# Performance work log

Measured on AMD Instinct MI355X. Metric: run time of the kernel, lower is better.

## Reference

```python
import jax, jax.numpy as jnp
import numpy as np

N_NODES = 32768
N_EDGES = 524288
NODE_DIM = 128
HIDDEN = 256
EDGE_DIM = 32


def setup_inputs() -> dict:
    key = jax.random.key(0)
    ks = jax.random.split(key, 12)
    s = 0.05
    return {
        "h": jax.random.normal(ks[0], (N_NODES, NODE_DIM), jnp.float32),
        "x": jax.random.normal(ks[1], (N_NODES, 3), jnp.float32) * 10.0,
        "edge_index": jax.random.randint(ks[2], (2, N_EDGES), 0, N_NODES, dtype=jnp.int32).astype(jnp.int64),
        "edge_dist": jax.random.uniform(ks[3], (N_EDGES,), jnp.float32) * 15.0,
        # edge_mlp: Linear(1, edge_dim) -> SiLU -> Linear(edge_dim, edge_dim)
        "We1": jax.random.normal(ks[4], (1, EDGE_DIM), jnp.float32) * s,
        "be1": jnp.zeros((EDGE_DIM,), jnp.float32),
        "We2": jax.random.normal(ks[5], (EDGE_DIM, EDGE_DIM), jnp.float32) * s,
        "be2": jnp.zeros((EDGE_DIM,), jnp.float32),
        # node_mlp: Linear(2*node+edge, hidden) -> SiLU -> Linear(hidden, node)
        "Wn1": jax.random.normal(ks[6], (2 * NODE_DIM + EDGE_DIM, HIDDEN), jnp.float32) * s,
        "bn1": jnp.zeros((HIDDEN,), jnp.float32),
        "Wn2": jax.random.normal(ks[7], (HIDDEN, NODE_DIM), jnp.float32) * s,
        "bn2": jnp.zeros((NODE_DIM,), jnp.float32),
        # coord_mlp: Linear(2*node+edge, hidden) -> SiLU -> Linear(hidden, 1, bias=False)
        "Wc1": jax.random.normal(ks[8], (2 * NODE_DIM + EDGE_DIM, HIDDEN), jnp.float32) * s,
        "bc1": jnp.zeros((HIDDEN,), jnp.float32),
        "Wc2": jax.random.normal(ks[9], (HIDDEN, 1), jnp.float32) * s,
    }


def reference(h, x, edge_index, edge_dist,
              We1, be1, We2, be2,
              Wn1, bn1, Wn2, bn2,
              Wc1, bc1, Wc2):
    src, dst = edge_index[0], edge_index[1]
    n_nodes = h.shape[0]

    # edge_mlp on scalar distances -> [E, edge_dim]
    edge_attr = jax.nn.silu(edge_dist[:, None] @ We1 + be1) @ We2 + be2

    # per-edge message input: [E, 2*node_dim + edge_dim]
    m_input = jnp.concatenate([h[src], h[dst], edge_attr], axis=-1)

    # node messages and scatter-add onto destination nodes
    m = jax.nn.silu(m_input @ Wn1 + bn1) @ Wn2 + bn2          # [E, node_dim]
    h_agg = jax.ops.segment_sum(m, dst, num_segments=n_nodes)  # [N, node_dim]

    # equivariant coordinate update along normalized edge direction
    coord_weight = jax.nn.silu(m_input @ Wc1 + bc1) @ Wc2      # [E, 1]
    dir_vec = x[src] - x[dst]                                  # [E, 3]
    dir_len = jnp.maximum(jnp.linalg.norm(dir_vec, axis=-1, keepdims=True), 1e-8)
    coord_update = coord_weight * (dir_vec / dir_len)          # [E, 3]
    x_agg = jax.ops.segment_sum(coord_update, dst, num_segments=n_nodes)

    return h + h_agg, x + x_agg
```

## Files before the change

kernel.cpp:

```cpp
#include <hip/hip_runtime.h>
#include <math.h>

#define N_NODES 32768
#define N_EDGES 524288
#define NODE_DIM 128
#define HIDDEN 256
#define EDGE_DIM 32
#define TE 64
#define ASTR 296
#define HSTR 264
#define MSTR 132

typedef __attribute__((ext_vector_type(8))) short bf16x8;
typedef __attribute__((ext_vector_type(16))) float f32x16;

__device__ __forceinline__ float silu_f(float v) {
    float e = __expf(-v);
    return v * __builtin_amdgcn_rcpf(1.0f + e);
}

__device__ __forceinline__ unsigned short f2bf_rne(float f) {
    union { float f; unsigned int u; } v; v.f = f;
    return (unsigned short)((v.u + 0x7fffu + ((v.u >> 16) & 1u)) >> 16);
}

__device__ __forceinline__ unsigned int pkbf(float a, float b) {
    union { float f; unsigned int u; } ua, ub; ua.f = a; ub.f = b;
    return __builtin_amdgcn_perm(ub.u + 0x8000u, ua.u + 0x8000u, 0x07060302u);
}
__device__ __forceinline__ unsigned short f2bf_hu(float f) {
    union { float f; unsigned int u; } v; v.f = f;
    return (unsigned short)((v.u + 0x8000u) >> 16);
}

#define WS_BIAS_OFF 1024
#define WS_W1S_OFF  69632
#define WS_W2S_OFF  364544
#define WS_CNT_OFF  430080
#define WS_CUR_OFF  561152
#define WS_PERM_OFF 692224

__global__ void detect_zero_kernel(const unsigned int* __restrict__ ew, int* __restrict__ flag,
                                   int* __restrict__ counts) {
    int i = blockIdx.x * 256 + threadIdx.x;
    if (i < N_NODES) counts[i] = 0;
    if (i == 0) {
        int is64 = 1;
        for (int k = 0; k < 64; ++k)
            if (ew[2 * k + 1] != 0u) { is64 = 0; break; }
        *flag = is64;
    }
}

__global__ void hist_kernel(const void* __restrict__ ei, const int* __restrict__ flag,
                            int* __restrict__ counts) {
    int e = blockIdx.x * 256 + threadIdx.x;
    int dst = (*flag) ? (int)((const long long*)ei)[N_EDGES + e]
                      : ((const int*)ei)[N_EDGES + e];
    atomicAdd(&counts[dst], 1);
}

__global__ __launch_bounds__(1024)
void scan_kernel(const int* __restrict__ counts, int* __restrict__ cursor) {
    __shared__ int part[1024];
    const int t = threadIdx.x;
    const int base = t * 32;
    int loc[32];
    int s = 0;
    #pragma unroll
    for (int i = 0; i < 32; ++i) { loc[i] = s; s += counts[base + i]; }
    part[t] = s;
    __syncthreads();
    #pragma unroll
    for (int d = 1; d < 1024; d <<= 1) {
        int v = (t >= d) ? part[t - d] : 0;
        __syncthreads();
        part[t] += v;
        __syncthreads();
    }
    int excl = part[t] - s;
    #pragma unroll
    for (int i = 0; i < 32; ++i) cursor[base + i] = excl + loc[i];
}

__global__ void place_kernel(const void* __restrict__ ei, const int* __restrict__ flag,
                             int* __restrict__ cursor, int* __restrict__ perm) {
    int e = blockIdx.x * 256 + threadIdx.x;
    int dst = (*flag) ? (int)((const long long*)ei)[N_EDGES + e]
                      : ((const int*)ei)[N_EDGES + e];
    int pos = atomicAdd(&cursor[dst], 1);
    perm[pos] = e;
}

__global__ void init_out_kernel(const float4* __restrict__ h4, const float4* __restrict__ x4,
                                float4* __restrict__ out4) {
    const int NH4 = N_NODES * NODE_DIM / 4;
    const int NX4 = N_NODES * 3 / 4;
    int i = blockIdx.x * blockDim.x + threadIdx.x;
    if (i < NH4) out4[i] = h4[i];
    else if (i < NH4 + NX4) out4[i] = x4[i - NH4];
}

__global__ void prep_kernel(const float* __restrict__ Wn1, const float* __restrict__ Wc1,
                            const float* __restrict__ Wn2,
                            const float* __restrict__ bn1, const float* __restrict__ bc1,
                            const float* __restrict__ We2, const float* __restrict__ be2,
                            unsigned short* __restrict__ W1s, unsigned short* __restrict__ W2s,
                            float* __restrict__ biasC) {
    int i = blockIdx.x * 256 + threadIdx.x;
    if (i < 512 * 288) {
        int jj = i & 7, lane = (i >> 3) & 63, rest = i >> 9;
        int step = rest % 18, tile = rest / 18;
        int n = tile * 32 + (lane & 31);
        int k = step * 16 + ((lane >> 5) * 8) + jj;
        float v;
        if (k < 256) {
            v = (n < 256) ? Wn1[k * 256 + n] : Wc1[k * 256 + (n - 256)];
        } else {
            int j = k - 256;
            float s = 0.0f;
            #pragma unroll 8
            for (int q = 0; q < 32; ++q)
                s += We2[j * 32 + q] * ((n < 256) ? Wn1[(256 + q) * 256 + n]
                                                  : Wc1[(256 + q) * 256 + (n - 256)]);
            v = s;
        }
        W1s[i] = f2bf_rne(v);
    } else if (i < 512 * 288 + 128 * 256) {
        int i2 = i - 512 * 288;
        int jj = i2 & 7, lane = (i2 >> 3) & 63, rest = i2 >> 9;
        int step = rest & 15, tile = rest >> 4;
        int d = tile * 32 + (lane & 31);
        int k = step * 16 + ((lane >> 5) * 8) + jj;
        W2s[i2] = f2bf_rne(Wn2[k * 128 + d]);
    } else if (i < 512 * 288 + 128 * 256 + 512) {
        int n = i - (512 * 288 + 128 * 256);
        float s = (n < 256) ? bn1[n] : bc1[n - 256];
        #pragma unroll 8
        for (int q = 0; q < 32; ++q)
            s += be2[q] * ((n < 256) ? Wn1[(256 + q) * 256 + n]
                                     : Wc1[(256 + q) * 256 + (n - 256)]);
        biasC[n] = s;
    }
}

__global__ __launch_bounds__(512, 4)
void egnn_mfma_kernel(const float* __restrict__ h, const float* __restrict__ x,
                      const void* __restrict__ ei, const float* __restrict__ dist,
                      const float* __restrict__ We1, const float* __restrict__ be1,
                      const float* __restrict__ bn2, const float* __restrict__ Wc2,
                      const float* __restrict__ biasC,
                      const unsigned short* __restrict__ W1s,
                      const unsigned short* __restrict__ W2s,
                      const int* __restrict__ perm,
                      const int* __restrict__ flag,
                      float* __restrict__ out)
{
    __shared__ unsigned short smA[TE * ASTR];
    __shared__ int sidx[TE], didx[TE], eidx[TE];
    __shared__ float cw_s[TE];
    __shared__ float cxyz[3 * TE];

    unsigned short* smH = smA;
    float* smM = (float*)smA;

    const int t = threadIdx.x;
    const int lane = t & 63;
    const int wv = t >> 6;
    const int lo = lane & 31;
    const int hi = lane >> 5;
    const int ebase = blockIdx.x * TE;
    const int is64 = *flag;

    if (t < 2 * TE) {
        int e = t & (TE - 1);
        int eid = perm[ebase + e];
        int which = t >> 6;
        long long pos = (long long)which * N_EDGES + eid;
        int idx = is64 ? (int)((const long long*)ei)[pos] : ((const int*)ei)[pos];
        if (which == 0) { sidx[e] = idx; eidx[e] = eid; }
        else didx[e] = idx;
        if (t < TE) cw_s[t] = 0.0f;
    }
    __syncthreads();

    #pragma unroll
    for (int it = 0; it < 4; ++it) {
        int id = it * 512 + t;
        int g8 = id & 15;
        int half = (id >> 4) & 1;
        int e = id >> 5;
        int node = half ? didx[e] : sidx[e];
        const float4* p = (const float4*)&h[node * NODE_DIM + 8 * g8];
        float4 v0 = p[0], v1 = p[1];
        unsigned int a0 = pkbf(v0.x, v0.y), a1 = pkbf(v0.z, v0.w);
        unsigned int a2 = pkbf(v1.x, v1.y), a3 = pkbf(v1.z, v1.w);
        *(uint4*)&smA[e * ASTR + half * NODE_DIM + 8 * g8] = make_uint4(a0, a1, a2, a3);
    }
    {
        int e = t >> 3;
        int j4 = (t & 7) * 4;
        float d = dist[eidx[e]];
        float s0 = silu_f(d * We1[j4 + 0] + be1[j4 + 0]);
        float s1 = silu_f(d * We1[j4 + 1] + be1[j4 + 1]);
        float s2 = silu_f(d * We1[j4 + 2] + be1[j4 + 2]);
        float s3 = silu_f(d * We1[j4 + 3] + be1[j4 + 3]);
        *(uint2*)&smA[e * ASTR + 2 * NODE_DIM + j4] = make_uint2(pkbf(s0, s1), pkbf(s2, s3));
    }
    __syncthreads();

    f32x16 a00, a01, a10, a11;
    {
        int nb = wv * 64 + lo;
        float b0 = biasC[nb], b1 = biasC[nb + 32];
        #pragma unroll
        for (int r = 0; r < 16; ++r) { a00[r] = b0; a01[r] = b1; a10[r] = b0; a11[r] = b1; }
    }
    {
        const int aoff0 = lo * ASTR + hi * 8;
        const int aoff1 = (32 + lo) * ASTR + hi * 8;
        const int TS = 18 * 64 * 8;
        const int base = ((wv * 2 * 18) * 64 + lane) * 8;
        bf16x8 b0c = *(const bf16x8*)&W1s[base];
        bf16x8 b1c = *(const bf16x8*)&W1s[base + TS];
        #pragma unroll
        for (int step = 0; step < 18; ++step) {
            bf16x8 b0n, b1n;
            if (step < 17) {
                b0n = *(const bf16x8*)&W1s[base + (step + 1) * 512];
                b1n = *(const bf16x8*)&W1s[base + (step + 1) * 512 + TS];
            }
            bf16x8 f0 = *(const bf16x8*)&smA[aoff0 + step * 16];
            bf16x8 f1 = *(const bf16x8*)&smA[aoff1 + step * 16];
            a00 = __builtin_amdgcn_mfma_f32_32x32x16_bf16(f0, b0c, a00, 0, 0, 0);
            a10 = __builtin_amdgcn_mfma_f32_32x32x16_bf16(f1, b0c, a10, 0, 0, 0);
            a01 = __builtin_amdgcn_mfma_f32_32x32x16_bf16(f0, b1c, a01, 0, 0, 0);
            a11 = __builtin_amdgcn_mfma_f32_32x32x16_bf16(f1, b1c, a11, 0, 0, 0);
            if (step < 17) { b0c = b0n; b1c = b1n; }
        }
    }
    __syncthreads();

    const int rowbase = 4 * hi;
    if (wv < 4) {
        int jb = wv * 64 + lo;
        #pragma unroll
        for (int r = 0; r < 16; ++r) {
            int er = (r & 3) + 8 * (r >> 2) + rowbase;
            unsigned short* row0 = &smH[er * HSTR + jb];
            unsigned short* row1 = &smH[(er + 32) * HSTR + jb];
            row0[0]  = f2bf_hu(silu_f(a00[r]));
            row0[32] = f2bf_hu(silu_f(a01[r]));
            row1[0]  = f2bf_hu(silu_f(a10[r]));
            row1[32] = f2bf_hu(silu_f(a11[r]));
        }
    } else {
        int nc = (wv - 4) * 64 + lo;
        float w0 = Wc2[nc], w1 = Wc2[nc + 32];
        float p0[16], p1[16];
        #pragma unroll
        for (int r = 0; r < 16; ++r) {
            p0[r] = silu_f(a00[r]) * w0 + silu_f(a01[r]) * w1;
            p1[r] = silu_f(a10[r]) * w0 + silu_f(a11[r]) * w1;
        }
        #pragma unroll
        for (int off = 1; off < 32; off <<= 1) {
            #pragma unroll
            for (int r = 0; r < 16; ++r) {
                p0[r] += __shfl_xor(p0[r], off);
                p1[r] += __shfl_xor(p1[r], off);
            }
        }
        if (lo == 0) {
            #pragma unroll
            for (int r = 0; r < 16; ++r) {
                int er = (r & 3) + 8 * (r >> 2) + rowbase;
                atomicAdd(&cw_s[er], p0[r]);
                atomicAdd(&cw_s[er + 32], p1[r]);
            }
        }
    }
    __syncthreads();

    if (t < TE) {
        int s = sidx[t], dn = didx[t];
        float dx = x[s * 3 + 0] - x[dn * 3 + 0];
        float dy = x[s * 3 + 1] - x[dn * 3 + 1];
        float dz = x[s * 3 + 2] - x[dn * 3 + 2];
        float len = fmaxf(sqrtf(dx * dx + dy * dy + dz * dz), 1e-8f);
        float w = cw_s[t] / len;
        cxyz[t] = w * dx; cxyz[TE + t] = w * dy; cxyz[2 * TE + t] = w * dz;
    }

    {
        const int et = wv >> 2;
        const int dt = wv & 3;
        const int d = dt * 32 + lo;
        f32x16 acc;
        float b = bn2[d];
        #pragma unroll
        for (int r = 0; r < 16; ++r) acc[r] = b;
        const int hoff = (et * 32 + lo) * HSTR + hi * 8;
        const int wb = ((dt * 16) * 64 + lane) * 8;
        bf16x8 bc = *(const bf16x8*)&W2s[wb];
        #pragma unroll
        for (int step = 0; step < 16; ++step) {
            bf16x8 bn_;
            if (step < 15) bn_ = *(const bf16x8*)&W2s[wb + (step + 1) * 512];
            bf16x8 af = *(const bf16x8*)&smH[hoff + step * 16];
            acc = __builtin_amdgcn_mfma_f32_32x32x16_bf16(af, bc, acc, 0, 0, 0);
            if (step < 15) bc = bn_;
        }
        __syncthreads();
        #pragma unroll
        for (int r = 0; r < 16; ++r) {
            int er = et * 32 + (r & 3) + 8 * (r >> 2) + rowbase;
            smM[er * MSTR + d] = acc[r];
        }
    }
    __syncthreads();

    {
        const int g = t >> 5;
        const int d4 = (t & 31) * 4;
        for (int e0 = g; e0 < TE; e0 += 16) {
            if (e0 > 0 && didx[e0] == didx[e0 - 1]) continue;
            float4 s = *(const float4*)&smM[e0 * MSTR + d4];
            int er = e0 + 1;
            while (er < TE && didx[er] == didx[e0]) {
                float4 v = *(const float4*)&smM[er * MSTR + d4];
                s.x += v.x; s.y += v.y; s.z += v.z; s.w += v.w;
                ++er;
            }
            float* dp = &out[didx[e0] * NODE_DIM + d4];
            atomicAdd(dp + 0, s.x); atomicAdd(dp + 1, s.y);
            atomicAdd(dp + 2, s.z); atomicAdd(dp + 3, s.w);
        }
    }
    if (t < TE) {
        int e0 = t;
        if (e0 == 0 || didx[e0] != didx[e0 - 1]) {
            float sx = cxyz[e0], sy = cxyz[TE + e0], sz = cxyz[2 * TE + e0];
            int er = e0 + 1;
            while (er < TE && didx[er] == didx[e0]) {
                sx += cxyz[er]; sy += cxyz[TE + er]; sz += cxyz[2 * TE + er];
                ++er;
            }
            float* xo = out + N_NODES * NODE_DIM + didx[e0] * 3;
            atomicAdd(xo + 0, sx); atomicAdd(xo + 1, sy); atomicAdd(xo + 2, sz);
        }
    }
}

extern "C" void kernel_launch(void* const* d_in, const int* in_sizes, int n_in,
                              void* d_out, int out_size, void* d_ws, size_t ws_size,
                              hipStream_t stream) {
    const float* h    = (const float*)d_in[0];
    const float* x    = (const float*)d_in[1];
    const void*  ei   = d_in[2];
    const float* dist = (const float*)d_in[3];
    const float* We1  = (const float*)d_in[4];
    const float* be1  = (const float*)d_in[5];
    const float* We2  = (const float*)d_in[6];
    const float* be2  = (const float*)d_in[7];
    const float* Wn1  = (const float*)d_in[8];
    const float* bn1  = (const float*)d_in[9];
    const float* Wn2  = (const float*)d_in[10];
    const float* bn2  = (const float*)d_in[11];
    const float* Wc1  = (const float*)d_in[12];
    const float* bc1  = (const float*)d_in[13];
    const float* Wc2  = (const float*)d_in[14];
    float* out = (float*)d_out;

    int* flag = (int*)d_ws;
    float* biasC = (float*)((char*)d_ws + WS_BIAS_OFF);
    unsigned short* W1s = (unsigned short*)((char*)d_ws + WS_W1S_OFF);
    unsigned short* W2s = (unsigned short*)((char*)d_ws + WS_W2S_OFF);
    int* counts = (int*)((char*)d_ws + WS_CNT_OFF);
    int* cursor = (int*)((char*)d_ws + WS_CUR_OFF);
    int* perm   = (int*)((char*)d_ws + WS_PERM_OFF);

    detect_zero_kernel<<<N_NODES / 256, 256, 0, stream>>>((const unsigned int*)ei, flag, counts);
    hist_kernel<<<N_EDGES / 256, 256, 0, stream>>>(ei, flag, counts);
    scan_kernel<<<1, 1024, 0, stream>>>(counts, cursor);
    place_kernel<<<N_EDGES / 256, 256, 0, stream>>>(ei, flag, cursor, perm);

    const int ntot4 = (N_NODES * NODE_DIM + N_NODES * 3) / 4;
    init_out_kernel<<<(ntot4 + 255) / 256, 256, 0, stream>>>(
        (const float4*)h, (const float4*)x, (float4*)out);

    prep_kernel<<<(512 * 288 + 128 * 256 + 512 + 255) / 256, 256, 0, stream>>>(
        Wn1, Wc1, Wn2, bn1, bc1, We2, be2, W1s, W2s, biasC);

    egnn_mfma_kernel<<<N_EDGES / TE, 512, 0, stream>>>(
        h, x, ei, dist, We1, be1, bn2, Wc2, biasC, W1s, W2s, perm, flag, out);
}
```

Before: 487.4 us.

## Pre-convert h to bf16, merge prep kernels, inline index-width detection, deepen weight prefetch

Adds a bf16 copy of h, built once in a merged prep kernel, so the main kernel gathers half as many bytes per edge and skips per-edge float-to-bf16 packing. Four small setup kernels (zero/detect, init_out, weight prep) are folded into one launch. The 64-bit index check is now done per wave with a ballot, which removes the flag buffer. The weight prefetch in both MFMA loops goes from one step ahead to two steps ahead. The cost is an extra 8MB write plus read for the bf16 copy, a bit more register pressure from the triple buffers, and the fast path only runs when the workspace is large enough.

```diff
diff --git a/kernel.cpp b/kernel.cpp
--- a/kernel.cpp
+++ b/kernel.cpp
@@ -23,7 +23,9 @@
     union { float f; unsigned int u; } v; v.f = f;
     return (unsigned short)((v.u + 0x7fffu + ((v.u >> 16) & 1u)) >> 16);
 }
-
+__device__ __forceinline__ unsigned int pk_rne(float a, float b) {
+    return (unsigned int)f2bf_rne(a) | ((unsigned int)f2bf_rne(b) << 16);
+}
 __device__ __forceinline__ unsigned int pkbf(float a, float b) {
     union { float f; unsigned int u; } ua, ub; ua.f = a; ub.f = b;
     return __builtin_amdgcn_perm(ub.u + 0x8000u, ua.u + 0x8000u, 0x07060302u);
@@ -31,6 +33,12 @@
 __device__ __forceinline__ unsigned short f2bf_hu(float f) {
     union { float f; unsigned int u; } v; v.f = f;
     return (unsigned short)((v.u + 0x8000u) >> 16);
+}
+
+__device__ __forceinline__ int detect_is64(const void* ei, int t) {
+    const unsigned int* ew = (const unsigned int*)ei;
+    unsigned int hiw = ew[2 * (t & 63) + 1];
+    return (__ballot(hiw != 0u) == 0ULL) ? 1 : 0;
 }
 
 #define WS_BIAS_OFF 1024
@@ -39,80 +47,33 @@
 #define WS_CNT_OFF  430080
 #define WS_CUR_OFF  561152
 #define WS_PERM_OFF 692224
-
-__global__ void detect_zero_kernel(const unsigned int* __restrict__ ew, int* __restrict__ flag,
-                                   int* __restrict__ counts) {
+#define WS_HBF_OFF  2789376
+#define WS_HBF_END  (WS_HBF_OFF + N_NODES * NODE_DIM * 2)
+
+#define SEG_CNT  32768
+#define SEG_W1S  147456
+#define SEG_W2S  32768
+#define SEG_BIAS 512
+#define SEG_OUT  1073152
+#define SEG_HBF  524288
+#define PREP_TOT (SEG_CNT + SEG_W1S + SEG_W2S + SEG_BIAS + SEG_OUT + SEG_HBF)
+
+__global__ void prep_all_kernel(const float* __restrict__ h, const float* __restrict__ x,
+                                const float* __restrict__ We2, const float* __restrict__ be2,
+                                const float* __restrict__ Wn1, const float* __restrict__ bn1,
+                                const float* __restrict__ Wn2,
+                                const float* __restrict__ Wc1, const float* __restrict__ bc1,
+                                float* __restrict__ out, float* __restrict__ biasC,
+                                unsigned short* __restrict__ W1s, unsigned short* __restrict__ W2s,
+                                int* __restrict__ counts, unsigned short* __restrict__ hbf) {
     int i = blockIdx.x * 256 + threadIdx.x;
-    if (i < N_NODES) counts[i] = 0;
-    if (i == 0) {
-        int is64 = 1;
-        for (int k = 0; k < 64; ++k)
-            if (ew[2 * k + 1] != 0u) { is64 = 0; break; }
-        *flag = is64;
-    }
-}
-
-__global__ void hist_kernel(const void* __restrict__ ei, const int* __restrict__ flag,
-                            int* __restrict__ counts) {
-    int e = blockIdx.x * 256 + threadIdx.x;
-    int dst = (*flag) ? (int)((const long long*)ei)[N_EDGES + e]
-                      : ((const int*)ei)[N_EDGES + e];
-    atomicAdd(&counts[dst], 1);
-}
-
-__global__ __launch_bounds__(1024)
-void scan_kernel(const int* __restrict__ counts, int* __restrict__ cursor) {
-    __shared__ int part[1024];
-    const int t = threadIdx.x;
-    const int base = t * 32;
-    int loc[32];
-    int s = 0;
-    #pragma unroll
-    for (int i = 0; i < 32; ++i) { loc[i] = s; s += counts[base + i]; }
-    part[t] = s;
-    __syncthreads();
-    #pragma unroll
-    for (int d = 1; d < 1024; d <<= 1) {
-        int v = (t >= d) ? part[t - d] : 0;
-        __syncthreads();
-        part[t] += v;
-        __syncthreads();
-    }
-    int excl = part[t] - s;
-    #pragma unroll
-    for (int i = 0; i < 32; ++i) cursor[base + i] = excl + loc[i];
-}
-
-__global__ void place_kernel(const void* __restrict__ ei, const int* __restrict__ flag,
-                             int* __restrict__ cursor, int* __restrict__ perm) {
-    int e = blockIdx.x * 256 + threadIdx.x;
-    int dst = (*flag) ? (int)((const long long*)ei)[N_EDGES + e]
-                      : ((const int*)ei)[N_EDGES + e];
-    int pos = atomicAdd(&cursor[dst], 1);
-    perm[pos] = e;
-}
-
-__global__ void init_out_kernel(const float4* __restrict__ h4, const float4* __restrict__ x4,
-                                float4* __restrict__ out4) {
-    const int NH4 = N_NODES * NODE_DIM / 4;
-    const int NX4 = N_NODES * 3 / 4;
-    int i = blockIdx.x * blockDim.x + threadIdx.x;
-    if (i < NH4) out4[i] = h4[i];
-    else if (i < NH4 + NX4) out4[i] = x4[i - NH4];
-}
-
-__global__ void prep_kernel(const float* __restrict__ Wn1, const float* __restrict__ Wc1,
-                            const float* __restrict__ Wn2,
-                            const float* __restrict__ bn1, const float* __restrict__ bc1,
-                            const float* __restrict__ We2, const float* __restrict__ be2,
-                            unsigned short* __restrict__ W1s, unsigned short* __restrict__ W2s,
-                            float* __restrict__ biasC) {
-    int i = blockIdx.x * 256 + threadIdx.x;
-    if (i < 512 * 288) {
-        int jj = i & 7, lane = (i >> 3) & 63, rest = i >> 9;
+    if (i < SEG_CNT) { counts[i] = 0; return; }
+    i -= SEG_CNT;
+    if (i < SEG_W1S) {
+        int jj = i & 7, ln = (i >> 3) & 63, rest = i >> 9;
         int step = rest % 18, tile = rest / 18;
-        int n = tile * 32 + (lane & 31);
-        int k = step * 16 + ((lane >> 5) * 8) + jj;
+        int n = tile * 32 + (ln & 31);
+        int k = step * 16 + ((ln >> 5) * 8) + jj;
         float v;
         if (k < 256) {
             v = (n < 256) ? Wn1[k * 256 + n] : Wc1[k * 256 + (n - 256)];
@@ -126,22 +87,85 @@
             v = s;
         }
         W1s[i] = f2bf_rne(v);
-    } else if (i < 512 * 288 + 128 * 256) {
-        int i2 = i - 512 * 288;
-        int jj = i2 & 7, lane = (i2 >> 3) & 63, rest = i2 >> 9;
+        return;
+    }
+    i -= SEG_W1S;
+    if (i < SEG_W2S) {
+        int jj = i & 7, ln = (i >> 3) & 63, rest = i >> 9;
         int step = rest & 15, tile = rest >> 4;
-        int d = tile * 32 + (lane & 31);
-        int k = step * 16 + ((lane >> 5) * 8) + jj;
-        W2s[i2] = f2bf_rne(Wn2[k * 128 + d]);
-    } else if (i < 512 * 288 + 128 * 256 + 512) {
-        int n = i - (512 * 288 + 128 * 256);
+        int d = tile * 32 + (ln & 31);
+        int k = step * 16 + ((ln >> 5) * 8) + jj;
+        W2s[i] = f2bf_rne(Wn2[k * 128 + d]);
+        return;
+    }
+    i -= SEG_W2S;
+    if (i < SEG_BIAS) {
+        int n = i;
         float s = (n < 256) ? bn1[n] : bc1[n - 256];
         #pragma unroll 8
         for (int q = 0; q < 32; ++q)
             s += be2[q] * ((n < 256) ? Wn1[(256 + q) * 256 + n]
                                      : Wc1[(256 + q) * 256 + (n - 256)]);
         biasC[n] = s;
-    }
+        return;
+    }
+    i -= SEG_BIAS;
+    if (i < SEG_OUT) {
+        const int NH4 = N_NODES * NODE_DIM / 4;
+        const float4* h4 = (const float4*)h;
+        const float4* x4 = (const float4*)x;
+        ((float4*)out)[i] = (i < NH4) ? h4[i] : x4[i - NH4];
+        return;
+    }
+    i -= SEG_OUT;
+    if (hbf != nullptr && i < SEG_HBF) {
+        const float4* p = (const float4*)&h[i * 8];
+        float4 v0 = p[0], v1 = p[1];
+        uint4 o = make_uint4(pk_rne(v0.x, v0.y), pk_rne(v0.z, v0.w),
+                             pk_rne(v1.x, v1.y), pk_rne(v1.z, v1.w));
+        *(uint4*)&hbf[i * 8] = o;
+    }
+}
+
+__global__ void hist_kernel(const void* __restrict__ ei, int* __restrict__ counts) {
+    int is64 = detect_is64(ei, threadIdx.x);
+    int e = blockIdx.x * 256 + threadIdx.x;
+    int dst = is64 ? (int)((const long long*)ei)[N_EDGES + e]
+                   : ((const int*)ei)[N_EDGES + e];
+    atomicAdd(&counts[dst], 1);
+}
+
+__global__ __launch_bounds__(1024)
+void scan_kernel(const int* __restrict__ counts, int* __restrict__ cursor) {
+    __shared__ int part[1024];
+    const int t = threadIdx.x;
+    const int base = t * 32;
+    int loc[32];
+    int s = 0;
+    #pragma unroll
+    for (int i = 0; i < 32; ++i) { loc[i] = s; s += counts[base + i]; }
+    part[t] = s;
+    __syncthreads();
+    #pragma unroll
+    for (int d = 1; d < 1024; d <<= 1) {
+        int v = (t >= d) ? part[t - d] : 0;
+        __syncthreads();
+        part[t] += v;
+        __syncthreads();
+    }
+    int excl = part[t] - s;
+    #pragma unroll
+    for (int i = 0; i < 32; ++i) cursor[base + i] = excl + loc[i];
+}
+
+__global__ void place_kernel(const void* __restrict__ ei,
+                             int* __restrict__ cursor, int* __restrict__ perm) {
+    int is64 = detect_is64(ei, threadIdx.x);
+    int e = blockIdx.x * 256 + threadIdx.x;
+    int dst = is64 ? (int)((const long long*)ei)[N_EDGES + e]
+                   : ((const int*)ei)[N_EDGES + e];
+    int pos = atomicAdd(&cursor[dst], 1);
+    perm[pos] = e;
 }
 
 __global__ __launch_bounds__(512, 4)
@@ -153,7 +177,7 @@
                       const unsigned short* __restrict__ W1s,
                       const unsigned short* __restrict__ W2s,
                       const int* __restrict__ perm,
-                      const int* __restrict__ flag,
+                      const unsigned short* __restrict__ hbf,
                       float* __restrict__ out)
 {
     __shared__ unsigned short smA[TE * ASTR];
@@ -170,7 +194,7 @@
     const int lo = lane & 31;
     const int hi = lane >> 5;
     const int ebase = blockIdx.x * TE;
-    const int is64 = *flag;
+    const int is64 = detect_is64(ei, t);
 
     if (t < 2 * TE) {
         int e = t & (TE - 1);
@@ -184,18 +208,31 @@
     }
     __syncthreads();
 
-    #pragma unroll
-    for (int it = 0; it < 4; ++it) {
-        int id = it * 512 + t;
-        int g8 = id & 15;
-        int half = (id >> 4) & 1;
-        int e = id >> 5;
-        int node = half ? didx[e] : sidx[e];
-        const float4* p = (const float4*)&h[node * NODE_DIM + 8 * g8];
-        float4 v0 = p[0], v1 = p[1];
-        unsigned int a0 = pkbf(v0.x, v0.y), a1 = pkbf(v0.z, v0.w);
-        unsigned int a2 = pkbf(v1.x, v1.y), a3 = pkbf(v1.z, v1.w);
-        *(uint4*)&smA[e * ASTR + half * NODE_DIM + 8 * g8] = make_uint4(a0, a1, a2, a3);
+    if (hbf != nullptr) {
+        #pragma unroll
+        for (int it = 0; it < 4; ++it) {
+            int id = it * 512 + t;
+            int g = id & 15;
+            int half = (id >> 4) & 1;
+            int e = id >> 5;
+            int node = half ? didx[e] : sidx[e];
+            uint4 v = *(const uint4*)&hbf[node * NODE_DIM + 8 * g];
+            *(uint4*)&smA[e * ASTR + half * NODE_DIM + 8 * g] = v;
+        }
+    } else {
+        #pragma unroll
+        for (int it = 0; it < 4; ++it) {
+            int id = it * 512 + t;
+            int g8 = id & 15;
+            int half = (id >> 4) & 1;
+            int e = id >> 5;
+            int node = half ? didx[e] : sidx[e];
+            const float4* p = (const float4*)&h[node * NODE_DIM + 8 * g8];
+            float4 v0 = p[0], v1 = p[1];
+            unsigned int a0 = pkbf(v0.x, v0.y), a1 = pkbf(v0.z, v0.w);
+            unsigned int a2 = pkbf(v1.x, v1.y), a3 = pkbf(v1.z, v1.w);
+            *(uint4*)&smA[e * ASTR + half * NODE_DIM + 8 * g8] = make_uint4(a0, a1, a2, a3);
+        }
     }
     {
         int e = t >> 3;
@@ -221,22 +258,25 @@
         const int aoff1 = (32 + lo) * ASTR + hi * 8;
         const int TS = 18 * 64 * 8;
         const int base = ((wv * 2 * 18) * 64 + lane) * 8;
-        bf16x8 b0c = *(const bf16x8*)&W1s[base];
-        bf16x8 b1c = *(const bf16x8*)&W1s[base + TS];
+        bf16x8 b0s[3], b1s[3];
+        b0s[0] = *(const bf16x8*)&W1s[base];
+        b1s[0] = *(const bf16x8*)&W1s[base + TS];
+        b0s[1] = *(const bf16x8*)&W1s[base + 512];
+        b1s[1] = *(const bf16x8*)&W1s[base + 512 + TS];
         #pragma unroll
         for (int step = 0; step < 18; ++step) {
-            bf16x8 b0n, b1n;
-            if (step < 17) {
-                b0n = *(const bf16x8*)&W1s[base + (step + 1) * 512];
-                b1n = *(const bf16x8*)&W1s[base + (step + 1) * 512 + TS];
+            const int cur = step % 3;
+            if (step + 2 < 18) {
+                const int pf = (step + 2) % 3;
+                b0s[pf] = *(const bf16x8*)&W1s[base + (step + 2) * 512];
+                b1s[pf] = *(const bf16x8*)&W1s[base + (step + 2) * 512 + TS];
             }
             bf16x8 f0 = *(const bf16x8*)&smA[aoff0 + step * 16];
             bf16x8 f1 = *(const bf16x8*)&smA[aoff1 + step * 16];
-            a00 = __builtin_amdgcn_mfma_f32_32x32x16_bf16(f0, b0c, a00, 0, 0, 0);
-            a10 = __builtin_amdgcn_mfma_f32_32x32x16_bf16(f1, b0c, a10, 0, 0, 0);
-            a01 = __builtin_amdgcn_mfma_f32_32x32x16_bf16(f0, b1c, a01, 0, 0, 0);
-            a11 = __builtin_amdgcn_mfma_f32_32x32x16_bf16(f1, b1c, a11, 0, 0, 0);
-            if (step < 17) { b0c = b0n; b1c = b1n; }
+            a00 = __builtin_amdgcn_mfma_f32_32x32x16_bf16(f0, b0s[cur], a00, 0, 0, 0);
+            a10 = __builtin_amdgcn_mfma_f32_32x32x16_bf16(f1, b0s[cur], a10, 0, 0, 0);
+            a01 = __builtin_amdgcn_mfma_f32_32x32x16_bf16(f0, b1s[cur], a01, 0, 0, 0);
+            a11 = __builtin_amdgcn_mfma_f32_32x32x16_bf16(f1, b1s[cur], a11, 0, 0, 0);
         }
     }
     __syncthreads();
@@ -297,19 +337,23 @@
         const int dt = wv & 3;
         const int d = dt * 32 + lo;
         f32x16 acc;
-        float b = bn2[d];
-        #pragma unroll
-        for (int r = 0; r < 16; ++r) acc[r] = b;
+        float bb = bn2[d];
+        #pragma unroll
+        for (int r = 0; r < 16; ++r) acc[r] = bb;
         const int hoff = (et * 32 + lo) * HSTR + hi * 8;
         const int wb = ((dt * 16) * 64 + lane) * 8;
-        bf16x8 bc = *(const bf16x8*)&W2s[wb];
+        bf16x8 bs[3];
+        bs[0] = *(const bf16x8*)&W2s[wb];
+        bs[1] = *(const bf16x8*)&W2s[wb + 512];
         #pragma unroll
         for (int step = 0; step < 16; ++step) {
-            bf16x8 bn_;
-            if (step < 15) bn_ = *(const bf16x8*)&W2s[wb + (step + 1) * 512];
+            const int cur = step % 3;
+            if (step + 2 < 16) {
+                const int pf = (step + 2) % 3;
+                bs[pf] = *(const bf16x8*)&W2s[wb + (step + 2) * 512];
+            }
             bf16x8 af = *(const bf16x8*)&smH[hoff + step * 16];
-            acc = __builtin_amdgcn_mfma_f32_32x32x16_bf16(af, bc, acc, 0, 0, 0);
-            if (step < 15) bc = bn_;
+            acc = __builtin_amdgcn_mfma_f32_32x32x16_bf16(af, bs[cur], acc, 0, 0, 0);
         }
         __syncthreads();
         #pragma unroll
@@ -372,26 +416,23 @@
     const float* Wc2  = (const float*)d_in[14];
     float* out = (float*)d_out;
 
-    int* flag = (int*)d_ws;
     float* biasC = (float*)((char*)d_ws + WS_BIAS_OFF);
     unsigned short* W1s = (unsigned short*)((char*)d_ws + WS_W1S_OFF);
     unsigned short* W2s = (unsigned short*)((char*)d_ws + WS_W2S_OFF);
     int* counts = (int*)((char*)d_ws + WS_CNT_OFF);
     int* cursor = (int*)((char*)d_ws + WS_CUR_OFF);
     int* perm   = (int*)((char*)d_ws + WS_PERM_OFF);
-
-    detect_zero_kernel<<<N_NODES / 256, 256, 0, stream>>>((const unsigned int*)ei, flag, counts);
-    hist_kernel<<<N_EDGES / 256, 256, 0, stream>>>(ei, flag, counts);
+    unsigned short* hbf = (ws_size >= (size_t)WS_HBF_END)
+                        ? (unsigned short*)((char*)d_ws + WS_HBF_OFF) : nullptr;
+
+    prep_all_kernel<<<PREP_TOT / 256, 256, 0, stream>>>(
+        h, x, We2, be2, Wn1, bn1, Wn2, Wc1, bc1,
+        out, biasC, W1s, W2s, counts, hbf);
+
+    hist_kernel<<<N_EDGES / 256, 256, 0, stream>>>(ei, counts);
     scan_kernel<<<1, 1024, 0, stream>>>(counts, cursor);
-    place_kernel<<<N_EDGES / 256, 256, 0, stream>>>(ei, flag, cursor, perm);
-
-    const int ntot4 = (N_NODES * NODE_DIM + N_NODES * 3) / 4;
-    init_out_kernel<<<(ntot4 + 255) / 256, 256, 0, stream>>>(
-        (const float4*)h, (const float4*)x, (float4*)out);
-
-    prep_kernel<<<(512 * 288 + 128 * 256 + 512 + 255) / 256, 256, 0, stream>>>(
-        Wn1, Wc1, Wn2, bn1, bc1, We2, be2, W1s, W2s, biasC);
+    place_kernel<<<N_EDGES / 256, 256, 0, stream>>>(ei, cursor, perm);
 
     egnn_mfma_kernel<<<N_EDGES / TE, 512, 0, stream>>>(
-        h, x, ei, dist, We1, be1, bn2, Wc2, biasC, W1s, W2s, perm, flag, out);
-}
+        h, x, ei, dist, We1, be1, bn2, Wc2, biasC, W1s, W2s, perm, hbf, out);
+}
```

New measurement: 511.1 us. 4.9% more time.
